# Optimization experiments

Hardware: AMD Instinct MI355X
Metric: run time of the kernel (lower is better)

The kernel has to match this reference:

```python
import jax, jax.numpy as jnp
import numpy as np

B = 65536
IN_DIM = 1280
E = 8          # num_experts
H1 = 256       # hidden_dim
H2 = 128       # hidden_dim // 2


def setup_inputs() -> dict:
    key = jax.random.key(0)
    ks = jax.random.split(key, 9)
    s1 = 1.0 / np.sqrt(IN_DIM)
    s2 = 1.0 / np.sqrt(H1)
    s3 = 1.0 / np.sqrt(H2)
    return {
        "x":  jax.random.normal(ks[0], (B, IN_DIM), dtype=jnp.float32),
        # stacked expert params: layer1 [E,in,H1], layer2 [E,H1,H2], layer3 [E,H2]
        "W1": jax.random.uniform(ks[1], (E, IN_DIM, H1), jnp.float32, -s1, s1),
        "b1": jax.random.uniform(ks[2], (E, H1), jnp.float32, -s1, s1),
        "W2": jax.random.uniform(ks[3], (E, H1, H2), jnp.float32, -s2, s2),
        "b2": jax.random.uniform(ks[4], (E, H2), jnp.float32, -s2, s2),
        "W3": jax.random.uniform(ks[5], (E, H2), jnp.float32, -s3, s3),
        "b3": jax.random.uniform(ks[6], (E,), jnp.float32, -s3, s3),
        # gate params [in,E]
        "Wg": jax.random.uniform(ks[7], (IN_DIM, E), jnp.float32, -s1, s1),
        "bg": jax.random.uniform(ks[8], (E,), jnp.float32, -s1, s1),
    }


def reference(x, W1, b1, W2, b2, W3, b3, Wg, bg):
    # All E experts run densely on every token (dropout = eval/identity).
    h1 = jax.nn.relu(jnp.einsum("bi,eih->beh", x, W1) + b1)          # [B,E,H1]
    h2 = jax.nn.relu(jnp.einsum("beh,ehk->bek", h1, W2) + b2)        # [B,E,H2]
    expert_out = jnp.einsum("bek,ek->be", h2, W3) + b3               # [B,E]
    gate = jax.nn.softmax(x @ Wg + bg, axis=-1)                      # [B,E]
    predictions = jnp.sum(expert_out * gate, axis=1)                 # [B]
    return predictions, gate
```

## Files before the change

kernel.cpp:

```cpp
#include <hip/hip_runtime.h>
#include <stdint.h>

#define NTOK 65536
#define KDIM 1280

typedef __attribute__((ext_vector_type(8))) short short8;
typedef __attribute__((ext_vector_type(4))) float floatx4;

__device__ __forceinline__ unsigned short f2bf(float f) {
  union { float f; unsigned int u; } v; v.f = f;
  unsigned int r = v.u + 0x7FFFu + ((v.u >> 16) & 1u);
  return (unsigned short)(r >> 16);
}
__device__ __forceinline__ float bf2f(unsigned int u16) {
  union { unsigned int u; float f; } v; v.u = u16 << 16; return v.f;
}

#define GLDS16(gp, lp) \
  __builtin_amdgcn_global_load_lds((const __attribute__((address_space(1))) void*)(gp), \
                                   (__attribute__((address_space(3))) void*)(lp), 16, 0, 0)


__global__ __launch_bounds__(256) void cast_x_kernel(const float4* __restrict__ x,
                                                     uint2* __restrict__ xb) {
  size_t i = (size_t)blockIdx.x * 256 + threadIdx.x;
  float4 v = x[i];
  uint2 o;
  o.x = (unsigned)f2bf(v.x) | ((unsigned)f2bf(v.y) << 16);
  o.y = (unsigned)f2bf(v.z) | ((unsigned)f2bf(v.w) << 16);
  xb[i] = o;
}

__global__ __launch_bounds__(256) void pack_w1_kernel(const float* __restrict__ W1,
                                                      unsigned short* __restrict__ W1t) {
  int t = blockIdx.x * 256 + threadIdx.x;
  if (t >= 2048 * 160) return;
  int n = t / 160, kg = t - n * 160;
  int e = n >> 8, h = n & 255;
  int k = kg * 8;
  const float* src = W1 + ((size_t)e * 1280 + k) * 256 + h;
  uint4 o;
  o.x = (unsigned)f2bf(src[0])       | ((unsigned)f2bf(src[256])     << 16);
  o.y = (unsigned)f2bf(src[2 * 256]) | ((unsigned)f2bf(src[3 * 256]) << 16);
  o.z = (unsigned)f2bf(src[4 * 256]) | ((unsigned)f2bf(src[5 * 256]) << 16);
  o.w = (unsigned)f2bf(src[6 * 256]) | ((unsigned)f2bf(src[7 * 256]) << 16);
  *(uint4*)(W1t + (size_t)n * 1280 + k) = o;
}

__global__ __launch_bounds__(256) void pack_w2_kernel(const float* __restrict__ W2,
                                                      unsigned short* __restrict__ W2t) {
  int t = blockIdx.x * 256 + threadIdx.x;
  if (t >= 1024 * 32) return;
  int ng = t >> 5, kg = t & 31;
  int e = ng >> 7, n = ng & 127;
  int k = kg * 8;
  const float* src = W2 + (size_t)e * 32768 + (size_t)k * 128 + n;
  uint4 o;
  o.x = (unsigned)f2bf(src[0])       | ((unsigned)f2bf(src[128])     << 16);
  o.y = (unsigned)f2bf(src[2 * 128]) | ((unsigned)f2bf(src[3 * 128]) << 16);
  o.z = (unsigned)f2bf(src[4 * 128]) | ((unsigned)f2bf(src[5 * 128]) << 16);
  o.w = (unsigned)f2bf(src[6 * 128]) | ((unsigned)f2bf(src[7 * 128]) << 16);
  *(uint4*)(W2t + (size_t)ng * 256 + k) = o;
}

__global__ __launch_bounds__(256) void pack_wg_kernel(const float* __restrict__ Wg,
                                                      unsigned short* __restrict__ WgTb) {
  int t = blockIdx.x * 256 + threadIdx.x;
  if (t >= 16 * 1280) return;
  int e = t / 1280, k = t - e * 1280;
  WgTb[t] = (e < 8) ? f2bf(Wg[(size_t)k * 8 + e]) : (unsigned short)0;
}


__global__ __launch_bounds__(256)
void gate_kernel(const unsigned short* __restrict__ xb,
                 const unsigned short* __restrict__ WgTb,
                 const float* __restrict__ bg,
                 float* __restrict__ outG) {
  __shared__ __align__(16) unsigned short WgL[16][1288];
  const int tid = threadIdx.x;
#pragma unroll
  for (int r = 0; r < 16; r++)
    if (tid < 160)
      *(uint4*)&WgL[r][tid * 8] = ((const uint4*)(WgTb + (size_t)r * 1280))[tid];
  __syncthreads();

  const int wv = tid >> 6, lane = tid & 63;
  const int fr = lane & 15;
  const int fkL = (lane >> 4) * 8;
  const int t0 = (blockIdx.x * 4 + wv) * 16;

  const unsigned short* arow = xb + (size_t)(t0 + fr) * 1280 + fkL;
  floatx4 acc = {0.f, 0.f, 0.f, 0.f};
  for (int k0 = 0; k0 < 1280; k0 += 32) {
    short8 af = *(const short8*)(arow + k0);
    short8 bf = *(const short8*)&WgL[fr][k0 + fkL];
    acc = __builtin_amdgcn_mfma_f32_16x16x32_bf16(af, bf, acc, 0, 0, 0);
  }
  const int ee = fr;
  float bgv = (ee < 8) ? bg[ee] : 0.f;
#pragma unroll
  for (int r = 0; r < 4; r++) {
    float v = acc[r] + bgv;
    float mx = v;
    mx = fmaxf(mx, __shfl_xor(mx, 1));
    mx = fmaxf(mx, __shfl_xor(mx, 2));
    mx = fmaxf(mx, __shfl_xor(mx, 4));
    float ex = __expf(v - mx);
    float s = ex;
    s += __shfl_xor(s, 1); s += __shfl_xor(s, 2); s += __shfl_xor(s, 4);
    float g = ex / s;
    if (ee < 8) outG[(size_t)(t0 + (lane >> 4) * 4 + r) * 8 + ee] = g;
  }
}


__global__ __launch_bounds__(256)
void expert_fused_kernel(const unsigned short* __restrict__ xb,
                         const unsigned short* __restrict__ W1t,
                         const float* __restrict__ b1,
                         const unsigned short* __restrict__ W2t,
                         const float* __restrict__ b2,
                         const float* __restrict__ W3,
                         const float* __restrict__ b3,
                         float* __restrict__ eo) {
  __shared__ __align__(16) unsigned short Ws[256 * 32];
  __shared__ __align__(16) unsigned short Xs[64 * 32];
  __shared__ __align__(16) unsigned short h1L[64 * 264];
  __shared__ float b1Ls[256];
  __shared__ float b2Ls[128];
  __shared__ float w3Ls[128];
  __shared__ float exS[4 * 64];

  const int tid = threadIdx.x;
  const int wv = tid >> 6;
  const int lane = tid & 63;
  const int e = blockIdx.x;
  const int m0 = blockIdx.y << 6;

  const unsigned short* W1te = W1t + (size_t)e * 256 * 1280;
  const unsigned short* W2te = W2t + (size_t)e * 128 * 256;

  b1Ls[tid] = b1[e * 256 + tid];
  if (tid < 128) { b2Ls[tid] = b2[e * 128 + tid]; w3Ls[tid] = W3[e * 128 + tid]; }

  const int lr = lane >> 2;
  const int ksw = ((lane & 3) ^ ((lane >> 3) & 3)) * 8;
  const int fr = lane & 15;
  const int fkS = (((lane >> 4) ^ ((lane >> 1) & 3)) & 3) * 8;
  const int fkL = (lane >> 4) * 8;
  const int rq = (lane >> 4) * 4;

  const unsigned short* gx = xb + (size_t)(m0 + wv * 16 + lr) * 1280 + ksw;
  const unsigned short* gw = W1te + (size_t)(wv * 64 + lr) * 1280 + ksw;
  unsigned short* lx = &Xs[(wv * 16) * 32];
  unsigned short* lw = &Ws[(wv * 64) * 32];

  floatx4 acc1[4][4] = {};
  for (int k0 = 0; k0 < 1280; k0 += 32) {
    GLDS16(gx + k0, lx);
    GLDS16(gw + k0, lw);
    GLDS16(gw + (size_t)16 * 1280 + k0, lw + 16 * 32);
    GLDS16(gw + (size_t)32 * 1280 + k0, lw + 32 * 32);
    GLDS16(gw + (size_t)48 * 1280 + k0, lw + 48 * 32);
    __syncthreads();
    short8 af[4], bfv[4];
#pragma unroll
    for (int i = 0; i < 4; i++)
      af[i] = *(const short8*)&Ws[(wv * 64 + i * 16 + fr) * 32 + fkS];
#pragma unroll
    for (int j = 0; j < 4; j++)
      bfv[j] = *(const short8*)&Xs[(j * 16 + fr) * 32 + fkS];
#pragma unroll
    for (int i = 0; i < 4; i++)
#pragma unroll
      for (int j = 0; j < 4; j++)
        acc1[i][j] = __builtin_amdgcn_mfma_f32_16x16x32_bf16(af[i], bfv[j], acc1[i][j], 0, 0, 0);
    __syncthreads();
  }

#pragma unroll
  for (int i = 0; i < 4; i++) {
    const int rowb = wv * 64 + i * 16 + rq;
    float bb0 = b1Ls[rowb], bb1 = b1Ls[rowb + 1], bb2 = b1Ls[rowb + 2], bb3 = b1Ls[rowb + 3];
#pragma unroll
    for (int j = 0; j < 4; j++) {
      float v0 = acc1[i][j][0] + bb0; v0 = v0 > 0.f ? v0 : 0.f;
      float v1 = acc1[i][j][1] + bb1; v1 = v1 > 0.f ? v1 : 0.f;
      float v2 = acc1[i][j][2] + bb2; v2 = v2 > 0.f ? v2 : 0.f;
      float v3 = acc1[i][j][3] + bb3; v3 = v3 > 0.f ? v3 : 0.f;
      uint2 pk;
      pk.x = (unsigned)f2bf(v0) | ((unsigned)f2bf(v1) << 16);
      pk.y = (unsigned)f2bf(v2) | ((unsigned)f2bf(v3) << 16);
      *(uint2*)&h1L[(j * 16 + fr) * 264 + rowb] = pk;
    }
  }
  __syncthreads();

  floatx4 acc2[2][4] = {};
  const unsigned short* gw2 = W2te + (size_t)(wv * 32 + lr) * 256 + ksw;
  unsigned short* lw2 = &Ws[(wv * 32) * 32];
  for (int k0 = 0; k0 < 256; k0 += 32) {
    GLDS16(gw2 + k0, lw2);
    GLDS16(gw2 + 16 * 256 + k0, lw2 + 16 * 32);
    __syncthreads();
    short8 a2[2], b2v[4];
#pragma unroll
    for (int i = 0; i < 2; i++)
      a2[i] = *(const short8*)&Ws[(wv * 32 + i * 16 + fr) * 32 + fkS];
#pragma unroll
    for (int j = 0; j < 4; j++)
      b2v[j] = *(const short8*)&h1L[(j * 16 + fr) * 264 + k0 + fkL];
#pragma unroll
    for (int i = 0; i < 2; i++)
#pragma unroll
      for (int j = 0; j < 4; j++)
        acc2[i][j] = __builtin_amdgcn_mfma_f32_16x16x32_bf16(a2[i], b2v[j], acc2[i][j], 0, 0, 0);
    __syncthreads();
  }

  float psum[4] = {0.f, 0.f, 0.f, 0.f};
#pragma unroll
  for (int i = 0; i < 2; i++) {
    const int rowb = wv * 32 + i * 16 + rq;
    float bb[4], ww[4];
#pragma unroll
    for (int r = 0; r < 4; r++) { bb[r] = b2Ls[rowb + r]; ww[r] = w3Ls[rowb + r]; }
#pragma unroll
    for (int j = 0; j < 4; j++)
#pragma unroll
      for (int r = 0; r < 4; r++) {
        float v = acc2[i][j][r] + bb[r];
        v = v > 0.f ? v : 0.f;
        psum[j] += v * ww[r];
      }
  }
#pragma unroll
  for (int j = 0; j < 4; j++) {
    float v = psum[j];
    v += __shfl_xor(v, 16);
    v += __shfl_xor(v, 32);
    psum[j] = v;
  }
  if (lane < 16) {
#pragma unroll
    for (int j = 0; j < 4; j++) exS[wv * 64 + j * 16 + lane] = psum[j];
  }
  __syncthreads();
  if (tid < 64) {
    float tot = exS[tid] + exS[64 + tid] + exS[128 + tid] + exS[192 + tid];
    eo[(size_t)(m0 + tid) * 8 + e] = tot + b3[e];
  }
}


__global__ __launch_bounds__(256)
void combine_kernel(const float* __restrict__ outG, const float* __restrict__ eo,
                    float* __restrict__ outP) {
  int t = blockIdx.x * 256 + threadIdx.x;
  const float4* g4 = (const float4*)(outG + (size_t)t * 8);
  const float4* e4 = (const float4*)(eo + (size_t)t * 8);
  float4 ga = g4[0], gb = g4[1], ea = e4[0], eb = e4[1];
  outP[t] = ga.x * ea.x + ga.y * ea.y + ga.z * ea.z + ga.w * ea.w +
            gb.x * eb.x + gb.y * eb.y + gb.z * eb.z + gb.w * eb.w;
}


extern "C" void kernel_launch(void* const* d_in, const int* in_sizes, int n_in,
                              void* d_out, int out_size, void* d_ws, size_t ws_size,
                              hipStream_t stream) {
  const float* x  = (const float*)d_in[0];
  const float* W1 = (const float*)d_in[1];
  const float* b1 = (const float*)d_in[2];
  const float* W2 = (const float*)d_in[3];
  const float* b2 = (const float*)d_in[4];
  const float* W3 = (const float*)d_in[5];
  const float* b3 = (const float*)d_in[6];
  const float* Wg = (const float*)d_in[7];
  const float* bg = (const float*)d_in[8];
  float* outP = (float*)d_out;
  float* outG = outP + NTOK;

  char* ws = (char*)d_ws;
  unsigned short* xb   = (unsigned short*)ws;
  unsigned short* W1t  = (unsigned short*)(ws + 167772160ll);
  unsigned short* W2t  = (unsigned short*)(ws + 173015040ll);
  unsigned short* WgTb = (unsigned short*)(ws + 173539328ll);
  float*          eo   = (float*)(ws + 173580288ll);

  cast_x_kernel<<<NTOK * KDIM / 4 / 256, 256, 0, stream>>>((const float4*)x, (uint2*)xb);
  pack_w1_kernel<<<1280, 256, 0, stream>>>(W1, W1t);
  pack_w2_kernel<<<128, 256, 0, stream>>>(W2, W2t);
  pack_wg_kernel<<<80, 256, 0, stream>>>(Wg, WgTb);

  gate_kernel<<<1024, 256, 0, stream>>>(xb, WgTb, bg, outG);
  expert_fused_kernel<<<dim3(8, 1024), 256, 0, stream>>>(xb, W1t, b1, W2t, b2, W3, b3, eo);
  combine_kernel<<<256, 256, 0, stream>>>(outG, eo, outP);
}
```

Measured before the change: 1.096 ms.

## Fuse gate GEMM and softmax into expert-0 blocks of the fused expert kernel

Removes the separate gate kernel, which reread all of xb, and computes the gate logits inside the expert-0 blocks by reusing the X tile already staged in LDS, with an extra MFMA per k-step and the softmax in the epilogue. Shared memory is merged into one buffer with aliased regions. The h1 tile now uses an XOR swizzle instead of row padding. The bias and W3 vectors are read straight from global memory instead of being staged in LDS. This saves a full pass over xb and one launch, at the cost of a small load imbalance for the expert-0 blocks and more aliasing complexity.

```diff
diff --git a/kernel.cpp b/kernel.cpp
--- a/kernel.cpp
+++ b/kernel.cpp
@@ -11,9 +11,6 @@
   union { float f; unsigned int u; } v; v.f = f;
   unsigned int r = v.u + 0x7FFFu + ((v.u >> 16) & 1u);
   return (unsigned short)(r >> 16);
-}
-__device__ __forceinline__ float bf2f(unsigned int u16) {
-  union { unsigned int u; float f; } v; v.u = u16 << 16; return v.f;
 }
 
 #define GLDS16(gp, lp) \
@@ -73,49 +70,6 @@
 
 
 __global__ __launch_bounds__(256)
-void gate_kernel(const unsigned short* __restrict__ xb,
-                 const unsigned short* __restrict__ WgTb,
-                 const float* __restrict__ bg,
-                 float* __restrict__ outG) {
-  __shared__ __align__(16) unsigned short WgL[16][1288];
-  const int tid = threadIdx.x;
-#pragma unroll
-  for (int r = 0; r < 16; r++)
-    if (tid < 160)
-      *(uint4*)&WgL[r][tid * 8] = ((const uint4*)(WgTb + (size_t)r * 1280))[tid];
-  __syncthreads();
-
-  const int wv = tid >> 6, lane = tid & 63;
-  const int fr = lane & 15;
-  const int fkL = (lane >> 4) * 8;
-  const int t0 = (blockIdx.x * 4 + wv) * 16;
-
-  const unsigned short* arow = xb + (size_t)(t0 + fr) * 1280 + fkL;
-  floatx4 acc = {0.f, 0.f, 0.f, 0.f};
-  for (int k0 = 0; k0 < 1280; k0 += 32) {
-    short8 af = *(const short8*)(arow + k0);
-    short8 bf = *(const short8*)&WgL[fr][k0 + fkL];
-    acc = __builtin_amdgcn_mfma_f32_16x16x32_bf16(af, bf, acc, 0, 0, 0);
-  }
-  const int ee = fr;
-  float bgv = (ee < 8) ? bg[ee] : 0.f;
-#pragma unroll
-  for (int r = 0; r < 4; r++) {
-    float v = acc[r] + bgv;
-    float mx = v;
-    mx = fmaxf(mx, __shfl_xor(mx, 1));
-    mx = fmaxf(mx, __shfl_xor(mx, 2));
-    mx = fmaxf(mx, __shfl_xor(mx, 4));
-    float ex = __expf(v - mx);
-    float s = ex;
-    s += __shfl_xor(s, 1); s += __shfl_xor(s, 2); s += __shfl_xor(s, 4);
-    float g = ex / s;
-    if (ee < 8) outG[(size_t)(t0 + (lane >> 4) * 4 + r) * 8 + ee] = g;
-  }
-}
-
-
-__global__ __launch_bounds__(256)
 void expert_fused_kernel(const unsigned short* __restrict__ xb,
                          const unsigned short* __restrict__ W1t,
                          const float* __restrict__ b1,
@@ -123,26 +77,25 @@
                          const float* __restrict__ b2,
                          const float* __restrict__ W3,
                          const float* __restrict__ b3,
+                         const unsigned short* __restrict__ WgTb,
+                         const float* __restrict__ bg,
+                         float* __restrict__ outG,
                          float* __restrict__ eo) {
-  __shared__ __align__(16) unsigned short Ws[256 * 32];
-  __shared__ __align__(16) unsigned short Xs[64 * 32];
-  __shared__ __align__(16) unsigned short h1L[64 * 264];
-  __shared__ float b1Ls[256];
-  __shared__ float b2Ls[128];
-  __shared__ float w3Ls[128];
-  __shared__ float exS[4 * 64];
+  __shared__ __align__(16) unsigned short smem[26624];
+  unsigned short* Ws  = smem;
+  unsigned short* Xs  = smem + 8192;
+  unsigned short* h1L = smem + 10240;
+  unsigned short* WgS = h1L;
 
   const int tid = threadIdx.x;
   const int wv = tid >> 6;
   const int lane = tid & 63;
   const int e = blockIdx.x;
   const int m0 = blockIdx.y << 6;
+  const bool gate_blk = (e == 0);
 
   const unsigned short* W1te = W1t + (size_t)e * 256 * 1280;
   const unsigned short* W2te = W2t + (size_t)e * 128 * 256;
-
-  b1Ls[tid] = b1[e * 256 + tid];
-  if (tid < 128) { b2Ls[tid] = b2[e * 128 + tid]; w3Ls[tid] = W3[e * 128 + tid]; }
 
   const int lr = lane >> 2;
   const int ksw = ((lane & 3) ^ ((lane >> 3) & 3)) * 8;
@@ -153,16 +106,20 @@
 
   const unsigned short* gx = xb + (size_t)(m0 + wv * 16 + lr) * 1280 + ksw;
   const unsigned short* gw = W1te + (size_t)(wv * 64 + lr) * 1280 + ksw;
+  const unsigned short* gwg = WgTb + (size_t)lr * 1280 + ksw;
   unsigned short* lx = &Xs[(wv * 16) * 32];
   unsigned short* lw = &Ws[(wv * 64) * 32];
+  const bool gate_stager = gate_blk && (wv == 0);
 
   floatx4 acc1[4][4] = {};
+  floatx4 accg = {0.f, 0.f, 0.f, 0.f};
   for (int k0 = 0; k0 < 1280; k0 += 32) {
     GLDS16(gx + k0, lx);
     GLDS16(gw + k0, lw);
     GLDS16(gw + (size_t)16 * 1280 + k0, lw + 16 * 32);
     GLDS16(gw + (size_t)32 * 1280 + k0, lw + 32 * 32);
     GLDS16(gw + (size_t)48 * 1280 + k0, lw + 48 * 32);
+    if (gate_stager) GLDS16(gwg + k0, WgS);
     __syncthreads();
     short8 af[4], bfv[4];
 #pragma unroll
@@ -176,23 +133,49 @@
 #pragma unroll
       for (int j = 0; j < 4; j++)
         acc1[i][j] = __builtin_amdgcn_mfma_f32_16x16x32_bf16(af[i], bfv[j], acc1[i][j], 0, 0, 0);
-    __syncthreads();
+    if (gate_blk) {
+      short8 ag = *(const short8*)&WgS[fr * 32 + fkS];
+      short8 bgf = *(const short8*)&Xs[(wv * 16 + fr) * 32 + fkS];
+      accg = __builtin_amdgcn_mfma_f32_16x16x32_bf16(ag, bgf, accg, 0, 0, 0);
+    }
+    __syncthreads();
+  }
+
+  if (gate_blk) {
+    const int g = lane >> 4;
+    float bg0 = 0.f, bg1 = 0.f, bg2 = 0.f, bg3 = 0.f;
+    if (g < 2) {
+      float4 t = *(const float4*)(bg + g * 4);
+      bg0 = t.x; bg1 = t.y; bg2 = t.z; bg3 = t.w;
+    }
+    float v0 = accg[0] + bg0, v1 = accg[1] + bg1, v2 = accg[2] + bg2, v3 = accg[3] + bg3;
+    float mx = fmaxf(fmaxf(v0, v1), fmaxf(v2, v3));
+    mx = fmaxf(mx, __shfl_xor(mx, 16));
+    float e0 = __expf(v0 - mx), e1 = __expf(v1 - mx), e2 = __expf(v2 - mx), e3 = __expf(v3 - mx);
+    float s = e0 + e1 + e2 + e3;
+    s += __shfl_xor(s, 16);
+    float inv = 1.f / s;
+    if (g < 2) {
+      float4 o; o.x = e0 * inv; o.y = e1 * inv; o.z = e2 * inv; o.w = e3 * inv;
+      *(float4*)&outG[(size_t)(m0 + wv * 16 + fr) * 8 + g * 4] = o;
+    }
   }
 
 #pragma unroll
   for (int i = 0; i < 4; i++) {
     const int rowb = wv * 64 + i * 16 + rq;
-    float bb0 = b1Ls[rowb], bb1 = b1Ls[rowb + 1], bb2 = b1Ls[rowb + 2], bb3 = b1Ls[rowb + 3];
+    const float4 bb = *(const float4*)(b1 + e * 256 + rowb);
 #pragma unroll
     for (int j = 0; j < 4; j++) {
-      float v0 = acc1[i][j][0] + bb0; v0 = v0 > 0.f ? v0 : 0.f;
-      float v1 = acc1[i][j][1] + bb1; v1 = v1 > 0.f ? v1 : 0.f;
-      float v2 = acc1[i][j][2] + bb2; v2 = v2 > 0.f ? v2 : 0.f;
-      float v3 = acc1[i][j][3] + bb3; v3 = v3 > 0.f ? v3 : 0.f;
+      float v0 = acc1[i][j][0] + bb.x; v0 = v0 > 0.f ? v0 : 0.f;
+      float v1 = acc1[i][j][1] + bb.y; v1 = v1 > 0.f ? v1 : 0.f;
+      float v2 = acc1[i][j][2] + bb.z; v2 = v2 > 0.f ? v2 : 0.f;
+      float v3 = acc1[i][j][3] + bb.w; v3 = v3 > 0.f ? v3 : 0.f;
       uint2 pk;
       pk.x = (unsigned)f2bf(v0) | ((unsigned)f2bf(v1) << 16);
       pk.y = (unsigned)f2bf(v2) | ((unsigned)f2bf(v3) << 16);
-      *(uint2*)&h1L[(j * 16 + fr) * 264 + rowb] = pk;
+      const int row = j * 16 + fr;
+      *(uint2*)((char*)h1L + ((row * 512 + rowb * 2) ^ ((row & 7) << 4))) = pk;
     }
   }
   __syncthreads();
@@ -209,8 +192,11 @@
     for (int i = 0; i < 2; i++)
       a2[i] = *(const short8*)&Ws[(wv * 32 + i * 16 + fr) * 32 + fkS];
 #pragma unroll
-    for (int j = 0; j < 4; j++)
-      b2v[j] = *(const short8*)&h1L[(j * 16 + fr) * 264 + k0 + fkL];
+    for (int j = 0; j < 4; j++) {
+      const int row = j * 16 + fr;
+      b2v[j] = *(const short8*)((const char*)h1L +
+               ((row * 512 + (k0 + fkL) * 2) ^ ((row & 7) << 4)));
+    }
 #pragma unroll
     for (int i = 0; i < 2; i++)
 #pragma unroll
@@ -223,16 +209,17 @@
 #pragma unroll
   for (int i = 0; i < 2; i++) {
     const int rowb = wv * 32 + i * 16 + rq;
-    float bb[4], ww[4];
-#pragma unroll
-    for (int r = 0; r < 4; r++) { bb[r] = b2Ls[rowb + r]; ww[r] = w3Ls[rowb + r]; }
+    const float4 bb = *(const float4*)(b2 + e * 128 + rowb);
+    const float4 ww = *(const float4*)(W3 + e * 128 + rowb);
+    const float bba[4] = {bb.x, bb.y, bb.z, bb.w};
+    const float wwa[4] = {ww.x, ww.y, ww.z, ww.w};
 #pragma unroll
     for (int j = 0; j < 4; j++)
 #pragma unroll
       for (int r = 0; r < 4; r++) {
-        float v = acc2[i][j][r] + bb[r];
+        float v = acc2[i][j][r] + bba[r];
         v = v > 0.f ? v : 0.f;
-        psum[j] += v * ww[r];
+        psum[j] += v * wwa[r];
       }
   }
 #pragma unroll
@@ -242,6 +229,7 @@
     v += __shfl_xor(v, 32);
     psum[j] = v;
   }
+  float* exS = (float*)Xs;
   if (lane < 16) {
 #pragma unroll
     for (int j = 0; j < 4; j++) exS[wv * 64 + j * 16 + lane] = psum[j];
@@ -293,7 +281,7 @@
   pack_w2_kernel<<<128, 256, 0, stream>>>(W2, W2t);
   pack_wg_kernel<<<80, 256, 0, stream>>>(Wg, WgTb);
 
-  gate_kernel<<<1024, 256, 0, stream>>>(xb, WgTb, bg, outG);
-  expert_fused_kernel<<<dim3(8, 1024), 256, 0, stream>>>(xb, W1t, b1, W2t, b2, W3, b3, eo);
+  expert_fused_kernel<<<dim3(8, 1024), 256, 0, stream>>>(xb, W1t, b1, W2t, b2, W3, b3,
+                                                         WgTb, bg, outG, eo);
   combine_kernel<<<256, 256, 0, stream>>>(outG, eo, outP);
 }
```

Result: no change. 1.077 ms (-1.7%).
